# Performance work log

Hardware: AMD Instinct MI355X
Metric: run time of the kernel (lower is better)

Reference implementation:

```python
import jax, jax.numpy as jnp
import numpy as np

D = 64          # feature dim
H_POS = 64      # pos_mlp hidden
H_ATTN = 4 * D  # attn_mlp hidden
B, N = 1, 1024


def setup_inputs() -> dict:
    key = jax.random.key(0)
    ks = jax.random.split(key, 12)
    s = lambda fan_in: 1.0 / np.sqrt(fan_in)
    return {
        "x": jax.random.normal(ks[0], (B, N, D), jnp.float32),
        "pos": jax.random.normal(ks[1], (B, N, 2), jnp.float32),
        "Wq": jax.random.normal(ks[2], (D, D), jnp.float32) * s(D),
        "Wk": jax.random.normal(ks[3], (D, D), jnp.float32) * s(D),
        "Wv": jax.random.normal(ks[4], (D, D), jnp.float32) * s(D),
        "pW1": jax.random.normal(ks[5], (2, H_POS), jnp.float32) * s(2),
        "pb1": jnp.zeros((H_POS,), jnp.float32),
        "pW2": jax.random.normal(ks[6], (H_POS, D), jnp.float32) * s(H_POS),
        "pb2": jnp.zeros((D,), jnp.float32),
        "aW1": jax.random.normal(ks[7], (D, H_ATTN), jnp.float32) * s(D),
        "ab1": jnp.zeros((H_ATTN,), jnp.float32),
        "aW2": jax.random.normal(ks[8], (H_ATTN, D), jnp.float32) * s(H_ATTN),
        "ab2": jnp.zeros((D,), jnp.float32),
    }


def reference(x, pos, Wq, Wk, Wv, pW1, pb1, pW2, pb2, aW1, ab1, aW2, ab2):
    # projections: [b, n, d]
    q = x @ Wq
    k = x @ Wk
    v = x @ Wv
    # pairwise relative positions: [b, i, j, 2]
    rel_pos = pos[:, :, None, :] - pos[:, None, :, :]
    # pos MLP: [b, i, j, d]
    rpe = jax.nn.relu(rel_pos @ pW1 + pb1) @ pW2 + pb2
    # pairwise q - k: [b, i, j, d]
    qk_rel = q[:, :, None, :] - k[:, None, :, :]
    # values broadcast over i, plus positional embedding: [b, i, j, d]
    vv = v[:, None, :, :] + rpe
    # attention MLP on (qk_rel + rpe): [b, i, j, d]
    sim = jax.nn.relu((qk_rel + rpe) @ aW1 + ab1) @ aW2 + ab2
    # softmax over j (axis=-2), per-channel
    attn = jax.nn.softmax(sim, axis=-2)
    # weighted aggregation: [b, i, d]
    agg = jnp.einsum('bijd,bijd->bid', attn, vv)
    return agg
```

## Files before the change

kernel.cpp:

```cpp
#include <hip/hip_runtime.h>


typedef float f32x4 __attribute__((ext_vector_type(4)));
using sh8 = __attribute__((ext_vector_type(8))) short;

static constexpr int NPTS = 1024;

static constexpr size_t BEXT_OFF = 0;
static constexpr size_t AW2F_OFF = 65536;
static constexpr size_t PW2F_OFF = 98304;
static constexpr size_t CARR_OFF = 106496;
static constexpr size_t AI_OFF   = 107520;
static constexpr size_t QI_OFF   = 369664;
static constexpr size_t VPT_OFF  = 631808;
static constexpr size_t AJ_OFF   = 893952;
static constexpr size_t KN_OFF   = 1025024;

__device__ __forceinline__ unsigned short f2b_rne(float f) {
    unsigned u = __float_as_uint(f);
    u += 0x7fffu + ((u >> 16) & 1u);
    return (unsigned short)(u >> 16);
}
__device__ __forceinline__ unsigned pk2(float lo, float hi) {
    return __builtin_amdgcn_perm(__float_as_uint(hi), __float_as_uint(lo), 0x07060302);
}
__device__ __forceinline__ float b2f(unsigned short s) {
    return __uint_as_float(((unsigned)s) << 16);
}

__global__ void prep_all(const float* __restrict__ x, const float* __restrict__ pos,
                         const float* __restrict__ Wq, const float* __restrict__ Wk,
                         const float* __restrict__ Wv, const float* __restrict__ pW1,
                         const float* __restrict__ pb1, const float* __restrict__ pW2,
                         const float* __restrict__ pb2, const float* __restrict__ aW1,
                         const float* __restrict__ ab1, const float* __restrict__ aW2,
                         unsigned short* __restrict__ bextf, unsigned short* __restrict__ aw2f,
                         unsigned short* __restrict__ pw2f, float* __restrict__ cArr,
                         float* __restrict__ qI, unsigned short* __restrict__ kN,
                         float* __restrict__ vPT, float* __restrict__ aI,
                         unsigned short* __restrict__ aJ)
{
    const int b = blockIdx.x;
    if (b < 209) {
        const int idx = b * 256 + threadIdx.x;
        if (idx < 32768) {
            const int k = idx >> 8, t = idx & 255;
            float val;
            if (k < 64) {
                float s = 0.f;
                for (int d = 0; d < 64; ++d) s = fmaf(pW2[k * 64 + d], aW1[d * 256 + t], s);
                val = s;
            } else {
                val = aW1[(k - 64) * 256 + t];
            }
            const int kc = k >> 5, kl = k & 31, qq = kl >> 3, e = kl & 7;
            const int ntg = t >> 4, tl = t & 15;
            bextf[(((size_t)(kc * 16 + ntg) * 64) + (qq * 16 + tl)) * 8 + e] = f2b_rne(val);
        } else if (idx < 49152) {
            const int r = idx - 32768;
            const int kp = r >> 6, d = r & 63;
            const int t = 64 * (kp >> 6) + 16 * (kp & 3) + ((kp >> 2) & 15);
            const int kc = kp >> 5, kl = kp & 31, qq = kl >> 3, e = kl & 7;
            const int nt = d >> 4, dl = d & 15;
            aw2f[(((size_t)(kc * 4 + nt) * 64) + (qq * 16 + dl)) * 8 + e] = f2b_rne(aW2[t * 64 + d]);
        } else if (idx < 53248) {
            const int r = idx - 49152;
            const int k = r >> 6, d = r & 63;
            const int kc = k >> 5, kl = k & 31, qq = kl >> 3, e = kl & 7;
            const int nt = d >> 4, dl = d & 15;
            pw2f[(((size_t)(kc * 4 + nt) * 64) + (qq * 16 + dl)) * 8 + e] = f2b_rne(pW2[k * 64 + d]);
        } else if (idx < 53504) {
            const int t = idx - 53248;
            float s = ab1[t];
            for (int d = 0; d < 64; ++d) s = fmaf(pb2[d], aW1[d * 256 + t], s);
            cArr[t] = s;
        }
    } else {
        const int t = threadIdx.x, sub = t >> 6, d = t & 63;
        const int i = (b - 209) * 4 + sub;
        __shared__ float xs[4][64];
        xs[sub][d] = x[i * 64 + d];
        __syncthreads();
        float q = 0.f, k = 0.f, v = 0.f;
        for (int e = 0; e < 64; ++e) {
            const float xe = xs[sub][e];
            q = fmaf(xe, Wq[e * 64 + d], q);
            k = fmaf(xe, Wk[e * 64 + d], k);
            v = fmaf(xe, Wv[e * 64 + d], v);
        }
        const float a = pos[i * 2] * pW1[d] + pos[i * 2 + 1] * pW1[64 + d];
        qI[i * 64 + d] = q;
        kN[i * 64 + d] = f2b_rne(-k);
        vPT[d * NPTS + i] = v + pb2[d];
        aI[i * 64 + d] = a + pb1[d];
        aJ[i * 64 + d] = f2b_rne(a);
    }
}

__global__ __launch_bounds__(256, 2) void ptl_main(
    const float* __restrict__ aI, const float* __restrict__ qI,
    const unsigned short* __restrict__ aJ, const unsigned short* __restrict__ kN,
    const float* __restrict__ vPT,
    const unsigned short* __restrict__ bextf, const unsigned short* __restrict__ aw2f,
    const unsigned short* __restrict__ pw2f, const float* __restrict__ cArr,
    float* __restrict__ out)
{
    const int i    = blockIdx.x;
    const int tid  = threadIdx.x;
    const int w    = tid >> 6;
    const int lane = tid & 63;
    const int m    = lane & 15;
    const int q    = lane >> 4;

    __shared__ __align__(16) uint4 AfL[2][2][4][64];
    __shared__ __align__(16) unsigned char Hs[2][2][16 * 528];

    sh8 Bf[16];
#pragma unroll
    for (int kc = 0; kc < 4; ++kc)
#pragma unroll
        for (int nt = 0; nt < 4; ++nt)
            Bf[kc * 4 + nt] = *(const sh8*)(bextf + ((size_t)((kc * 16 + 4 * w + nt) * 64 + lane)) * 8);
    sh8 W2f[8];
#pragma unroll
    for (int kc = 0; kc < 8; ++kc)
        W2f[kc] = *(const sh8*)(aw2f + ((size_t)((kc * 4 + w) * 64 + lane)) * 8);
    sh8 P2f[2];
#pragma unroll
    for (int kc = 0; kc < 2; ++kc)
        P2f[kc] = *(const sh8*)(pw2f + ((size_t)((kc * 4 + w) * 64 + lane)) * 8);

    f32x4 cvec[4];
#pragma unroll
    for (int nt = 0; nt < 4; ++nt) {
        const float c = cArr[64 * w + 16 * nt + m];
        cvec[nt] = (f32x4){c, c, c, c};
    }

    const int  half   = w & 1;
    const bool isRelu = (w < 2);
    const unsigned short* bsrc  = (isRelu ? aJ : kN) + m * 64 + half * 32 + q * 8;
    const float*          ibase = (isRelu ? aI : qI) + i * 64 + half * 32 + q * 8;
    float iv[8];
    *(float4*)(iv)     = *(const float4*)(ibase);
    *(float4*)(iv + 4) = *(const float4*)(ibase + 4);

#pragma unroll
    for (int s = 0; s < 2; ++s) {
        const sh8 raw = *(const sh8*)(bsrc + (size_t)(16 * s) * 64);
        float t[8];
#pragma unroll
        for (int e = 0; e < 8; ++e)
            t[e] = isRelu ? fmaxf(iv[e] - b2f((unsigned short)raw[e]), 0.f)
                          : iv[e] + b2f((unsigned short)raw[e]);
        uint4 pk;
        pk.x = pk2(t[0], t[1]); pk.y = pk2(t[2], t[3]);
        pk.z = pk2(t[4], t[5]); pk.w = pk2(t[6], t[7]);
        AfL[0][s][w][lane] = pk;
    }
    __syncthreads();

    float num = 0.f, den = 0.f;
    const f32x4 z4 = {0.f, 0.f, 0.f, 0.f};
    const float* vbase = vPT + (size_t)(16 * w + m) * NPTS;

    for (int n = 0; n < 32; ++n) {
        const int pb = n & 1, nb = pb ^ 1;
        const int j0 = n << 5;

        sh8 raw0, raw1;
        if (n < 31) {
            raw0 = *(const sh8*)(bsrc + (size_t)(j0 + 32) * 64);
            raw1 = *(const sh8*)(bsrc + (size_t)(j0 + 48) * 64);
        }
        const float4 vj0 = *(const float4*)(vbase + j0 + 4 * q);
        const float4 vj1 = *(const float4*)(vbase + j0 + 16 + 4 * q);

        const sh8 A00 = *(const sh8*)&AfL[pb][0][0][lane];
        const sh8 A01 = *(const sh8*)&AfL[pb][0][1][lane];
        const sh8 A02 = *(const sh8*)&AfL[pb][0][2][lane];
        const sh8 A03 = *(const sh8*)&AfL[pb][0][3][lane];
        {
            f32x4 acc[4];
#pragma unroll
            for (int nt = 0; nt < 4; ++nt) {
                acc[nt] = __builtin_amdgcn_mfma_f32_16x16x32_bf16(A00, Bf[0 * 4 + nt], cvec[nt], 0, 0, 0);
                acc[nt] = __builtin_amdgcn_mfma_f32_16x16x32_bf16(A01, Bf[1 * 4 + nt], acc[nt], 0, 0, 0);
                acc[nt] = __builtin_amdgcn_mfma_f32_16x16x32_bf16(A02, Bf[2 * 4 + nt], acc[nt], 0, 0, 0);
                acc[nt] = __builtin_amdgcn_mfma_f32_16x16x32_bf16(A03, Bf[3 * 4 + nt], acc[nt], 0, 0, 0);
            }
            unsigned char* hw = Hs[pb][0] + (4 * q) * 528 + 128 * w + 8 * m;
#pragma unroll
            for (int r = 0; r < 4; ++r) {
                uint2 pk;
                pk.x = pk2(fmaxf(acc[0][r], 0.f), fmaxf(acc[1][r], 0.f));
                pk.y = pk2(fmaxf(acc[2][r], 0.f), fmaxf(acc[3][r], 0.f));
                *(uint2*)(hw + r * 528) = pk;
            }
        }

        const sh8 A10 = *(const sh8*)&AfL[pb][1][0][lane];
        const sh8 A11 = *(const sh8*)&AfL[pb][1][1][lane];
        const sh8 A12 = *(const sh8*)&AfL[pb][1][2][lane];
        const sh8 A13 = *(const sh8*)&AfL[pb][1][3][lane];
        {
            f32x4 acc[4];
#pragma unroll
            for (int nt = 0; nt < 4; ++nt) {
                acc[nt] = __builtin_amdgcn_mfma_f32_16x16x32_bf16(A10, Bf[0 * 4 + nt], cvec[nt], 0, 0, 0);
                acc[nt] = __builtin_amdgcn_mfma_f32_16x16x32_bf16(A11, Bf[1 * 4 + nt], acc[nt], 0, 0, 0);
                acc[nt] = __builtin_amdgcn_mfma_f32_16x16x32_bf16(A12, Bf[2 * 4 + nt], acc[nt], 0, 0, 0);
                acc[nt] = __builtin_amdgcn_mfma_f32_16x16x32_bf16(A13, Bf[3 * 4 + nt], acc[nt], 0, 0, 0);
            }
            unsigned char* hw = Hs[pb][1] + (4 * q) * 528 + 128 * w + 8 * m;
#pragma unroll
            for (int r = 0; r < 4; ++r) {
                uint2 pk;
                pk.x = pk2(fmaxf(acc[0][r], 0.f), fmaxf(acc[1][r], 0.f));
                pk.y = pk2(fmaxf(acc[2][r], 0.f), fmaxf(acc[3][r], 0.f));
                *(uint2*)(hw + r * 528) = pk;
            }
        }

        if (n < 31) {
#pragma unroll
            for (int s = 0; s < 2; ++s) {
                const sh8 raw = s ? raw1 : raw0;
                float t[8];
#pragma unroll
                for (int e = 0; e < 8; ++e)
                    t[e] = isRelu ? fmaxf(iv[e] - b2f((unsigned short)raw[e]), 0.f)
                                  : iv[e] + b2f((unsigned short)raw[e]);
                uint4 pk;
                pk.x = pk2(t[0], t[1]); pk.y = pk2(t[2], t[3]);
                pk.z = pk2(t[4], t[5]); pk.w = pk2(t[6], t[7]);
                AfL[nb][s][w][lane] = pk;
            }
        }

        __syncthreads();

        {
            f32x4 accS = z4;
#pragma unroll
            for (int kc = 0; kc < 8; ++kc) {
                const sh8 hf = *(const sh8*)(Hs[pb][0] + m * 528 + kc * 64 + 16 * q);
                accS = __builtin_amdgcn_mfma_f32_16x16x32_bf16(hf, W2f[kc], accS, 0, 0, 0);
            }
            const f32x4 vc = {vj0.x, vj0.y, vj0.z, vj0.w};
            f32x4 accR = __builtin_amdgcn_mfma_f32_16x16x32_bf16(A00, P2f[0], vc, 0, 0, 0);
            accR = __builtin_amdgcn_mfma_f32_16x16x32_bf16(A01, P2f[1], accR, 0, 0, 0);
#pragma unroll
            for (int r = 0; r < 4; ++r) {
                const float ex = __expf(accS[r]);
                num = fmaf(ex, accR[r], num);
                den += ex;
            }
        }
        {
            f32x4 accS = z4;
#pragma unroll
            for (int kc = 0; kc < 8; ++kc) {
                const sh8 hf = *(const sh8*)(Hs[pb][1] + m * 528 + kc * 64 + 16 * q);
                accS = __builtin_amdgcn_mfma_f32_16x16x32_bf16(hf, W2f[kc], accS, 0, 0, 0);
            }
            const f32x4 vc = {vj1.x, vj1.y, vj1.z, vj1.w};
            f32x4 accR = __builtin_amdgcn_mfma_f32_16x16x32_bf16(A10, P2f[0], vc, 0, 0, 0);
            accR = __builtin_amdgcn_mfma_f32_16x16x32_bf16(A11, P2f[1], accR, 0, 0, 0);
#pragma unroll
            for (int r = 0; r < 4; ++r) {
                const float ex = __expf(accS[r]);
                num = fmaf(ex, accR[r], num);
                den += ex;
            }
        }
    }

    num += __shfl_xor(num, 16);
    num += __shfl_xor(num, 32);
    den += __shfl_xor(den, 16);
    den += __shfl_xor(den, 32);
    if (q == 0) out[i * 64 + 16 * w + m] = num / den;
}

extern "C" void kernel_launch(void* const* d_in, const int* in_sizes, int n_in,
                              void* d_out, int out_size, void* d_ws, size_t ws_size,
                              hipStream_t stream) {
    const float* x   = (const float*)d_in[0];
    const float* pos = (const float*)d_in[1];
    const float* Wq  = (const float*)d_in[2];
    const float* Wk  = (const float*)d_in[3];
    const float* Wv  = (const float*)d_in[4];
    const float* pW1 = (const float*)d_in[5];
    const float* pb1 = (const float*)d_in[6];
    const float* pW2 = (const float*)d_in[7];
    const float* pb2 = (const float*)d_in[8];
    const float* aW1 = (const float*)d_in[9];
    const float* ab1 = (const float*)d_in[10];
    const float* aW2 = (const float*)d_in[11];

    char* ws = (char*)d_ws;
    unsigned short* bextf = (unsigned short*)(ws + BEXT_OFF);
    unsigned short* aw2f  = (unsigned short*)(ws + AW2F_OFF);
    unsigned short* pw2f  = (unsigned short*)(ws + PW2F_OFF);
    float*          cArr  = (float*)(ws + CARR_OFF);
    float*          aIa   = (float*)(ws + AI_OFF);
    float*          qIa   = (float*)(ws + QI_OFF);
    float*          vPTa  = (float*)(ws + VPT_OFF);
    unsigned short* aJa   = (unsigned short*)(ws + AJ_OFF);
    unsigned short* kNa   = (unsigned short*)(ws + KN_OFF);

    prep_all<<<465, 256, 0, stream>>>(x, pos, Wq, Wk, Wv, pW1, pb1, pW2, pb2, aW1, ab1, aW2,
                                      bextf, aw2f, pw2f, cArr, qIa, kNa, vPTa, aIa, aJa);
    ptl_main<<<NPTS, 256, 0, stream>>>(aIa, qIa, aJa, kNa, vPTa, bextf, aw2f, pw2f, cArr,
                                       (float*)d_out);
}
```

Before: 193.0 us.

## Run second attention MLP matmul in FP8 with scaled MFMA and exp2

```diff
diff --git a/kernel.cpp b/kernel.cpp
--- a/kernel.cpp
+++ b/kernel.cpp
@@ -2,6 +2,7 @@
 
 
 typedef float f32x4 __attribute__((ext_vector_type(4)));
+typedef int   i32x8 __attribute__((ext_vector_type(8)));
 using sh8 = __attribute__((ext_vector_type(8))) short;
 
 static constexpr int NPTS = 1024;
@@ -27,6 +28,22 @@
 __device__ __forceinline__ float b2f(unsigned short s) {
     return __uint_as_float(((unsigned)s) << 16);
 }
+__device__ __forceinline__ unsigned char f2fp8(float v) {
+    return (unsigned char)(__builtin_amdgcn_cvt_pk_fp8_f32(v, 0.f, 0, false) & 0xff);
+}
+__device__ __forceinline__ unsigned pk4fp8(float a, float b, float c, float d) {
+    int r = __builtin_amdgcn_cvt_pk_fp8_f32(a, b, 0, false);
+    r = __builtin_amdgcn_cvt_pk_fp8_f32(c, d, r, true);
+    return (unsigned)r;
+}
+__device__ __forceinline__ i32x8 ld32B(const void* p) {
+    const uint4 a = ((const uint4*)p)[0];
+    const uint4 b = ((const uint4*)p)[1];
+    i32x8 r;
+    r[0] = a.x; r[1] = a.y; r[2] = a.z; r[3] = a.w;
+    r[4] = b.x; r[5] = b.y; r[6] = b.z; r[7] = b.w;
+    return r;
+}
 
 __global__ void prep_all(const float* __restrict__ x, const float* __restrict__ pos,
                          const float* __restrict__ Wq, const float* __restrict__ Wk,
@@ -34,7 +51,7 @@
                          const float* __restrict__ pb1, const float* __restrict__ pW2,
                          const float* __restrict__ pb2, const float* __restrict__ aW1,
                          const float* __restrict__ ab1, const float* __restrict__ aW2,
-                         unsigned short* __restrict__ bextf, unsigned short* __restrict__ aw2f,
+                         unsigned short* __restrict__ bextf, unsigned char* __restrict__ aw2f8,
                          unsigned short* __restrict__ pw2f, float* __restrict__ cArr,
                          float* __restrict__ qI, unsigned short* __restrict__ kN,
                          float* __restrict__ vPT, float* __restrict__ aI,
@@ -58,11 +75,12 @@
             bextf[(((size_t)(kc * 16 + ntg) * 64) + (qq * 16 + tl)) * 8 + e] = f2b_rne(val);
         } else if (idx < 49152) {
             const int r = idx - 32768;
-            const int kp = r >> 6, d = r & 63;
+            const int e = r & 31, lane = (r >> 5) & 63, wsl = (r >> 11) & 3, kb = r >> 13;
+            const int q = lane >> 4, dl = lane & 15;
+            const int kp = kb * 128 + q * 32 + e;
             const int t = 64 * (kp >> 6) + 16 * (kp & 3) + ((kp >> 2) & 15);
-            const int kc = kp >> 5, kl = kp & 31, qq = kl >> 3, e = kl & 7;
-            const int nt = d >> 4, dl = d & 15;
-            aw2f[(((size_t)(kc * 4 + nt) * 64) + (qq * 16 + dl)) * 8 + e] = f2b_rne(aW2[t * 64 + d]);
+            const int d = 16 * wsl + dl;
+            aw2f8[r] = f2fp8(aW2[t * 64 + d] * 1.4426950408889634f);
         } else if (idx < 53248) {
             const int r = idx - 49152;
             const int k = r >> 6, d = r & 63;
@@ -101,7 +119,7 @@
     const float* __restrict__ aI, const float* __restrict__ qI,
     const unsigned short* __restrict__ aJ, const unsigned short* __restrict__ kN,
     const float* __restrict__ vPT,
-    const unsigned short* __restrict__ bextf, const unsigned short* __restrict__ aw2f,
+    const unsigned short* __restrict__ bextf, const unsigned char* __restrict__ aw2f8,
     const unsigned short* __restrict__ pw2f, const float* __restrict__ cArr,
     float* __restrict__ out)
 {
@@ -113,7 +131,7 @@
     const int q    = lane >> 4;
 
     __shared__ __align__(16) uint4 AfL[2][2][4][64];
-    __shared__ __align__(16) unsigned char Hs[2][2][16 * 528];
+    __shared__ __align__(16) unsigned char Hs[2][2][16 * 272];
 
     sh8 Bf[16];
 #pragma unroll
@@ -121,21 +139,18 @@
 #pragma unroll
         for (int nt = 0; nt < 4; ++nt)
             Bf[kc * 4 + nt] = *(const sh8*)(bextf + ((size_t)((kc * 16 + 4 * w + nt) * 64 + lane)) * 8);
-    sh8 W2f[8];
-#pragma unroll
-    for (int kc = 0; kc < 8; ++kc)
-        W2f[kc] = *(const sh8*)(aw2f + ((size_t)((kc * 4 + w) * 64 + lane)) * 8);
+    i32x8 W2f[2];
+#pragma unroll
+    for (int kb = 0; kb < 2; ++kb)
+        W2f[kb] = ld32B(aw2f8 + ((size_t)((kb * 4 + w) * 64 + lane)) * 32);
     sh8 P2f[2];
 #pragma unroll
     for (int kc = 0; kc < 2; ++kc)
         P2f[kc] = *(const sh8*)(pw2f + ((size_t)((kc * 4 + w) * 64 + lane)) * 8);
 
-    f32x4 cvec[4];
-#pragma unroll
-    for (int nt = 0; nt < 4; ++nt) {
-        const float c = cArr[64 * w + 16 * nt + m];
-        cvec[nt] = (f32x4){c, c, c, c};
-    }
+    float creg[4];
+#pragma unroll
+    for (int nt = 0; nt < 4; ++nt) creg[nt] = cArr[64 * w + 16 * nt + m];
 
     const int  half   = w & 1;
     const bool isRelu = (w < 2);
@@ -184,19 +199,17 @@
             f32x4 acc[4];
 #pragma unroll
             for (int nt = 0; nt < 4; ++nt) {
-                acc[nt] = __builtin_amdgcn_mfma_f32_16x16x32_bf16(A00, Bf[0 * 4 + nt], cvec[nt], 0, 0, 0);
+                const f32x4 cv = {creg[nt], creg[nt], creg[nt], creg[nt]};
+                acc[nt] = __builtin_amdgcn_mfma_f32_16x16x32_bf16(A00, Bf[0 * 4 + nt], cv, 0, 0, 0);
                 acc[nt] = __builtin_amdgcn_mfma_f32_16x16x32_bf16(A01, Bf[1 * 4 + nt], acc[nt], 0, 0, 0);
                 acc[nt] = __builtin_amdgcn_mfma_f32_16x16x32_bf16(A02, Bf[2 * 4 + nt], acc[nt], 0, 0, 0);
                 acc[nt] = __builtin_amdgcn_mfma_f32_16x16x32_bf16(A03, Bf[3 * 4 + nt], acc[nt], 0, 0, 0);
             }
-            unsigned char* hw = Hs[pb][0] + (4 * q) * 528 + 128 * w + 8 * m;
-#pragma unroll
-            for (int r = 0; r < 4; ++r) {
-                uint2 pk;
-                pk.x = pk2(fmaxf(acc[0][r], 0.f), fmaxf(acc[1][r], 0.f));
-                pk.y = pk2(fmaxf(acc[2][r], 0.f), fmaxf(acc[3][r], 0.f));
-                *(uint2*)(hw + r * 528) = pk;
-            }
+            unsigned char* hw = Hs[pb][0] + (4 * q) * 272 + 64 * w + 4 * m;
+#pragma unroll
+            for (int r = 0; r < 4; ++r)
+                *(unsigned*)(hw + r * 272) = pk4fp8(fmaxf(acc[0][r], 0.f), fmaxf(acc[1][r], 0.f),
+                                                   fmaxf(acc[2][r], 0.f), fmaxf(acc[3][r], 0.f));
         }
 
         const sh8 A10 = *(const sh8*)&AfL[pb][1][0][lane];
@@ -207,19 +220,17 @@
             f32x4 acc[4];
 #pragma unroll
             for (int nt = 0; nt < 4; ++nt) {
-                acc[nt] = __builtin_amdgcn_mfma_f32_16x16x32_bf16(A10, Bf[0 * 4 + nt], cvec[nt], 0, 0, 0);
+                const f32x4 cv = {creg[nt], creg[nt], creg[nt], creg[nt]};
+                acc[nt] = __builtin_amdgcn_mfma_f32_16x16x32_bf16(A10, Bf[0 * 4 + nt], cv, 0, 0, 0);
                 acc[nt] = __builtin_amdgcn_mfma_f32_16x16x32_bf16(A11, Bf[1 * 4 + nt], acc[nt], 0, 0, 0);
                 acc[nt] = __builtin_amdgcn_mfma_f32_16x16x32_bf16(A12, Bf[2 * 4 + nt], acc[nt], 0, 0, 0);
                 acc[nt] = __builtin_amdgcn_mfma_f32_16x16x32_bf16(A13, Bf[3 * 4 + nt], acc[nt], 0, 0, 0);
             }
-            unsigned char* hw = Hs[pb][1] + (4 * q) * 528 + 128 * w + 8 * m;
-#pragma unroll
-            for (int r = 0; r < 4; ++r) {
-                uint2 pk;
-                pk.x = pk2(fmaxf(acc[0][r], 0.f), fmaxf(acc[1][r], 0.f));
-                pk.y = pk2(fmaxf(acc[2][r], 0.f), fmaxf(acc[3][r], 0.f));
-                *(uint2*)(hw + r * 528) = pk;
-            }
+            unsigned char* hw = Hs[pb][1] + (4 * q) * 272 + 64 * w + 4 * m;
+#pragma unroll
+            for (int r = 0; r < 4; ++r)
+                *(unsigned*)(hw + r * 272) = pk4fp8(fmaxf(acc[0][r], 0.f), fmaxf(acc[1][r], 0.f),
+                                                   fmaxf(acc[2][r], 0.f), fmaxf(acc[3][r], 0.f));
         }
 
         if (n < 31) {
@@ -240,39 +251,31 @@
 
         __syncthreads();
 
-        {
-            f32x4 accS = z4;
-#pragma unroll
-            for (int kc = 0; kc < 8; ++kc) {
-                const sh8 hf = *(const sh8*)(Hs[pb][0] + m * 528 + kc * 64 + 16 * q);
-                accS = __builtin_amdgcn_mfma_f32_16x16x32_bf16(hf, W2f[kc], accS, 0, 0, 0);
-            }
-            const f32x4 vc = {vj0.x, vj0.y, vj0.z, vj0.w};
-            f32x4 accR = __builtin_amdgcn_mfma_f32_16x16x32_bf16(A00, P2f[0], vc, 0, 0, 0);
-            accR = __builtin_amdgcn_mfma_f32_16x16x32_bf16(A01, P2f[1], accR, 0, 0, 0);
-#pragma unroll
-            for (int r = 0; r < 4; ++r) {
-                const float ex = __expf(accS[r]);
-                num = fmaf(ex, accR[r], num);
-                den += ex;
-            }
-        }
-        {
-            f32x4 accS = z4;
-#pragma unroll
-            for (int kc = 0; kc < 8; ++kc) {
-                const sh8 hf = *(const sh8*)(Hs[pb][1] + m * 528 + kc * 64 + 16 * q);
-                accS = __builtin_amdgcn_mfma_f32_16x16x32_bf16(hf, W2f[kc], accS, 0, 0, 0);
-            }
-            const f32x4 vc = {vj1.x, vj1.y, vj1.z, vj1.w};
-            f32x4 accR = __builtin_amdgcn_mfma_f32_16x16x32_bf16(A10, P2f[0], vc, 0, 0, 0);
-            accR = __builtin_amdgcn_mfma_f32_16x16x32_bf16(A11, P2f[1], accR, 0, 0, 0);
-#pragma unroll
-            for (int r = 0; r < 4; ++r) {
-                const float ex = __expf(accS[r]);
-                num = fmaf(ex, accR[r], num);
-                den += ex;
-            }
+        f32x4 aS0 = z4, aS1 = z4;
+#pragma unroll
+        for (int kb = 0; kb < 2; ++kb) {
+            const i32x8 h0 = ld32B(Hs[pb][0] + m * 272 + kb * 128 + 32 * q);
+            aS0 = __builtin_amdgcn_mfma_scale_f32_16x16x128_f8f6f4(
+                h0, W2f[kb], aS0, 0, 0, 0, 127, 0, 127);
+            const i32x8 h1 = ld32B(Hs[pb][1] + m * 272 + kb * 128 + 32 * q);
+            aS1 = __builtin_amdgcn_mfma_scale_f32_16x16x128_f8f6f4(
+                h1, W2f[kb], aS1, 0, 0, 0, 127, 0, 127);
+        }
+        const f32x4 vc0 = {vj0.x, vj0.y, vj0.z, vj0.w};
+        const f32x4 vc1 = {vj1.x, vj1.y, vj1.z, vj1.w};
+        f32x4 aR0 = __builtin_amdgcn_mfma_f32_16x16x32_bf16(A00, P2f[0], vc0, 0, 0, 0);
+        aR0 = __builtin_amdgcn_mfma_f32_16x16x32_bf16(A01, P2f[1], aR0, 0, 0, 0);
+        f32x4 aR1 = __builtin_amdgcn_mfma_f32_16x16x32_bf16(A10, P2f[0], vc1, 0, 0, 0);
+        aR1 = __builtin_amdgcn_mfma_f32_16x16x32_bf16(A11, P2f[1], aR1, 0, 0, 0);
+
+#pragma unroll
+        for (int r = 0; r < 4; ++r) {
+            const float e0 = exp2f(aS0[r]);
+            num = fmaf(e0, aR0[r], num);
+            den += e0;
+            const float e1 = exp2f(aS1[r]);
+            num = fmaf(e1, aR1[r], num);
+            den += e1;
         }
     }
 
@@ -301,7 +304,7 @@
 
     char* ws = (char*)d_ws;
     unsigned short* bextf = (unsigned short*)(ws + BEXT_OFF);
-    unsigned short* aw2f  = (unsigned short*)(ws + AW2F_OFF);
+    unsigned char*  aw2f8 = (unsigned char*)(ws + AW2F_OFF);
     unsigned short* pw2f  = (unsigned short*)(ws + PW2F_OFF);
     float*          cArr  = (float*)(ws + CARR_OFF);
     float*          aIa   = (float*)(ws + AI_OFF);
@@ -311,7 +314,7 @@
     unsigned short* kNa   = (unsigned short*)(ws + KN_OFF);
 
     prep_all<<<465, 256, 0, stream>>>(x, pos, Wq, Wk, Wv, pW1, pb1, pW2, pb2, aW1, ab1, aW2,
-                                      bextf, aw2f, pw2f, cArr, qIa, kNa, vPTa, aIa, aJa);
-    ptl_main<<<NPTS, 256, 0, stream>>>(aIa, qIa, aJa, kNa, vPTa, bextf, aw2f, pw2f, cArr,
+                                      bextf, aw2f8, pw2f, cArr, qIa, kNa, vPTa, aIa, aJa);
+    ptl_main<<<NPTS, 256, 0, stream>>>(aIa, qIa, aJa, kNa, vPTa, bextf, aw2f8, pw2f, cArr,
                                        (float*)d_out);
 }
```

After: 189.7 us. About the same (-1.7%).
